# Optimization experiments

Hardware: AMD Instinct MI355X
Metric: run time of the kernel (lower is better)

## Reference

```python
import jax, jax.numpy as jnp
import numpy as np

HIDDEN_DIM = 640
VOCAB_SIZE = 1024


def setup_inputs() -> dict:
    key = jax.random.key(0)
    kf, kp, kw, kb = jax.random.split(key, 4)
    B, T, U, H, V = 8, 256, 64, HIDDEN_DIM, VOCAB_SIZE
    f = jax.random.normal(kf, (B, T, H), dtype=jnp.float32)
    p = jax.random.normal(kp, (B, U, H), dtype=jnp.float32)
    # nn.Linear default init: U(-1/sqrt(H), 1/sqrt(H))
    bound = 1.0 / np.sqrt(H)
    W = jax.random.uniform(kw, (V, H), minval=-bound, maxval=bound, dtype=jnp.float32)
    b = jax.random.uniform(kb, (V,), minval=-bound, maxval=bound, dtype=jnp.float32)
    return {"f": f, "p": p, "W": W, "b": b}


def reference(f, p, W, b):
    # f: (B,T,H), p: (B,U,H) -> combined: (B,T,U,H)
    combined = f[:, :, None, :] + p[:, None, :, :]
    h = jax.nn.relu(combined)
    # Linear: h @ W^T + b -> (B,T,U,V)
    logits = jnp.einsum('btuh,vh->btuv', h, W) + b
    return logits
```

## Files before the change

### kernel.cpp

```cpp
#include <hip/hip_runtime.h>
#include <hip/hip_bf16.h>

#define BDIM 8
#define TDIM 256
#define UDIM 64
#define HDIM 640
#define VDIM 1024
#define MDIM (BDIM * TDIM * UDIM)

#define BM 128
#define BN 128
#define BK 32
#define NT (HDIM / BK)

typedef __attribute__((ext_vector_type(8))) short short8;
typedef __attribute__((ext_vector_type(4))) float f32x4;

__device__ __forceinline__ ushort f2bf(float x) {
    union { float f; unsigned int u; } v; v.f = x;
    unsigned int r = (v.u + 0x7fffu + ((v.u >> 16) & 1u)) >> 16;
    return (ushort)r;
}

__global__ void cvt_w_kernel(const float* __restrict__ W, ushort* __restrict__ Wb) {
    int i = (blockIdx.x * 256 + threadIdx.x) * 4;
    f32x4 w = *(const f32x4*)(W + i);
    ushort4 o;
    o.x = f2bf(w[0]); o.y = f2bf(w[1]); o.z = f2bf(w[2]); o.w = f2bf(w[3]);
    *(ushort4*)(Wb + i) = o;
}

__global__ __launch_bounds__(256) void build_h_kernel(
    const float* __restrict__ f, const float* __restrict__ p,
    ushort* __restrict__ h)
{
    const int tid = threadIdx.x;
    const int row = (blockIdx.x << 5) + (tid >> 3);
    const int j0  = tid & 7;
    const int b = row >> 14;
    const int t = (row >> 6) & (TDIM - 1);
    const int u = row & (UDIM - 1);
    const float* frow = f + (size_t)(b * TDIM + t) * HDIM;
    const float* prow = p + (size_t)(b * UDIM + u) * HDIM;
    ushort* hrow = h + (size_t)row * HDIM;
    #pragma unroll
    for (int it = 0; it < HDIM / 64; ++it) {
        const int k = (j0 + it * 8) * 8;
        f32x4 f0 = *(const f32x4*)(frow + k);
        f32x4 f1 = *(const f32x4*)(frow + k + 4);
        f32x4 p0 = *(const f32x4*)(prow + k);
        f32x4 p1 = *(const f32x4*)(prow + k + 4);
        short8 hv;
        #pragma unroll
        for (int e = 0; e < 4; ++e) {
            float a0 = fmaxf(f0[e] + p0[e], 0.0f);
            float a1 = fmaxf(f1[e] + p1[e], 0.0f);
            hv[e]     = (short)f2bf(a0);
            hv[e + 4] = (short)f2bf(a1);
        }
        *(short8*)(hrow + k) = hv;
    }
}

#define GLDS(srcptr, ldsptr)                                                   \
    __builtin_amdgcn_global_load_lds(                                          \
        (const __attribute__((address_space(1))) void*)(srcptr),               \
        (__attribute__((address_space(3))) void*)(ldsptr), 16, 0, 0)

__global__ __launch_bounds__(256, 4) void hgemm128_kernel(
    const ushort* __restrict__ h,
    const ushort* __restrict__ Wb,
    const float* __restrict__ bias,
    float* __restrict__ out)
{
    __shared__ ushort Ash[2][BM * BK];
    __shared__ ushort Bsh[2][BN * BK];

    const int tid  = threadIdx.x;
    const int lane = tid & 63;
    const int wave = tid >> 6;
    const int wm   = wave >> 1;
    const int wn   = wave & 1;

    const int bid   = blockIdx.x;
    const int work  = (bid & 7) * 1024 + (bid >> 3);
    const int mtile = work >> 3;
    const int ntile = work & 7;
    const int m0 = mtile * BM;
    const int v0 = ntile * BN;

    const ushort* hbase = h  + (size_t)m0 * HDIM;
    const ushort* wbase = Wb + (size_t)v0 * HDIM;

    const int r0a = tid >> 2;
    const int r0b = r0a + 64;
    const int j0  = tid & 3;
    const size_t sof0 = (size_t)r0a * HDIM + (j0 ^ ((r0a >> 1) & 3)) * 8;
    const size_t sof1 = (size_t)r0b * HDIM + (j0 ^ ((r0b >> 1) & 3)) * 8;
    const int u0 = (wave * 64) * 8;
    const int u1 = (256 + wave * 64) * 8;

    int aoff[4], boff[4];
    #pragma unroll
    for (int mi = 0; mi < 4; ++mi) {
        const int r = wm * 64 + mi * 16 + (lane & 15);
        aoff[mi] = (r * 4 + ((lane >> 4) ^ ((r >> 1) & 3))) * 8;
    }
    #pragma unroll
    for (int ni = 0; ni < 4; ++ni) {
        const int r = wn * 64 + ni * 16 + (lane & 15);
        boff[ni] = (r * 4 + ((lane >> 4) ^ ((r >> 1) & 3))) * 8;
    }

    f32x4 acc[4][4];
    #pragma unroll
    for (int i = 0; i < 4; ++i)
        #pragma unroll
        for (int j = 0; j < 4; ++j)
            acc[i][j] = (f32x4)0.0f;

#define STG(kt, bf) do {                                                       \
        GLDS(hbase + sof0 + (kt) * BK, &Ash[bf][u0]);                          \
        GLDS(hbase + sof1 + (kt) * BK, &Ash[bf][u1]);                          \
        GLDS(wbase + sof0 + (kt) * BK, &Bsh[bf][u0]);                          \
        GLDS(wbase + sof1 + (kt) * BK, &Bsh[bf][u1]);                          \
    } while (0)

#define TILE(t, d) do {                                                        \
        if ((t) + 1 < NT) {                                                    \
            STG((t) + 1, (d) ^ 1);                                             \
            asm volatile("s_waitcnt vmcnt(4)" ::: "memory");                   \
        } else {                                                               \
            asm volatile("s_waitcnt vmcnt(0)" ::: "memory");                   \
        }                                                                      \
        __builtin_amdgcn_sched_barrier(0);                                     \
        __builtin_amdgcn_s_barrier();         \
        __builtin_amdgcn_sched_barrier(0);                                     \
        short8 afr[4], bfr[4];                                                 \
        _Pragma("unroll")                                                      \
        for (int q = 0; q < 4; ++q) {                                          \
            afr[q] = *(const short8*)(&Ash[d][aoff[q]]);                       \
            bfr[q] = *(const short8*)(&Bsh[d][boff[q]]);                       \
        }                                                                      \
        __builtin_amdgcn_s_setprio(1);                                         \
        _Pragma("unroll")                                                      \
        for (int mi = 0; mi < 4; ++mi)                                         \
            _Pragma("unroll")                                                  \
            for (int ni = 0; ni < 4; ++ni)                                     \
                acc[mi][ni] = __builtin_amdgcn_mfma_f32_16x16x32_bf16(         \
                    afr[mi], bfr[ni], acc[mi][ni], 0, 0, 0);                   \
        __builtin_amdgcn_s_setprio(0);                                         \
        __builtin_amdgcn_sched_barrier(0);                                     \
        __builtin_amdgcn_s_barrier();              \
    } while (0)

    STG(0, 0);
    #pragma unroll 1
    for (int t = 0; t < NT; t += 2) {
        TILE(t, 0);
        TILE(t + 1, 1);
    }
#undef TILE
#undef STG

    #pragma unroll
    for (int ni = 0; ni < 4; ++ni) {
        const int col = v0 + wn * 64 + ni * 16 + (lane & 15);
        const float bv = bias[col];
        #pragma unroll
        for (int mi = 0; mi < 4; ++mi) {
            const int rbase = m0 + wm * 64 + mi * 16 + ((lane >> 4) << 2);
            #pragma unroll
            for (int reg = 0; reg < 4; ++reg) {
                out[(size_t)(rbase + reg) * VDIM + col] = acc[mi][ni][reg] + bv;
            }
        }
    }
}

template <bool USE_WB>
__global__ __launch_bounds__(256) void joint_gemm_kernel(
    const float* __restrict__ f, const float* __restrict__ p,
    const float* __restrict__ Wf, const ushort* __restrict__ Wb,
    const float* __restrict__ bias, float* __restrict__ out)
{
    __shared__ ushort Alds[128 * 64];
    __shared__ ushort Blds[128 * 64];

    const int tid  = threadIdx.x;
    const int lane = tid & 63;
    const int wave = tid >> 6;
    const int wm   = wave >> 1;
    const int wn   = wave & 1;

    const int bid   = blockIdx.x;
    const int work  = (bid & 7) * 1024 + (bid >> 3);
    const int mtile = work >> 3;
    const int ntile = work & 7;
    const int m0 = mtile * 128;
    const int v0 = ntile * 128;

    const int b  = m0 >> 14;
    const int t0 = (m0 >> 6) & (TDIM - 1);

    const float*  fbase = f + (size_t)(b * TDIM + t0) * HDIM;
    const float*  pbase = p + (size_t)b * UDIM * HDIM;
    const ushort* wbbase = Wb + (size_t)v0 * HDIM;
    const float*  wfbase = Wf + (size_t)v0 * HDIM;

    f32x4 acc[4][4];
    #pragma unroll
    for (int i = 0; i < 4; ++i)
        #pragma unroll
        for (int j = 0; j < 4; ++j)
            acc[i][j] = (f32x4)0.0f;

    for (int kt = 0; kt < HDIM / 64; ++kt) {
        const int k0 = kt * 64;
        __syncthreads();

        if (USE_WB) {
            #pragma unroll
            for (int it = 0; it < 4; ++it) {
                const int c   = it * 256 + tid;
                const int row = c >> 3;
                const int j   = c & 7;
                const ushort* src = wbbase + row * HDIM + k0 + ((j ^ (row & 7)) << 3);
                GLDS(src, &Blds[(it * 256 + wave * 64) * 8]);
            }
        } else {
            #pragma unroll
            for (int it = 0; it < 4; ++it) {
                const int c   = it * 256 + tid;
                const int row = c >> 3;
                const int j   = c & 7;
                const float* wp = wfbase + row * HDIM + k0 + j * 8;
                f32x4 w0 = *(const f32x4*)wp;
                f32x4 w1 = *(const f32x4*)(wp + 4);
                short8 wv;
                #pragma unroll
                for (int e = 0; e < 4; ++e) {
                    wv[e]     = (short)f2bf(w0[e]);
                    wv[e + 4] = (short)f2bf(w1[e]);
                }
                *(short8*)(&Blds[(row * 8 + (j ^ (row & 7))) * 8]) = wv;
            }
        }

        #pragma unroll
        for (int it = 0; it < 4; ++it) {
            const int c   = it * 256 + tid;
            const int row = c >> 3;
            const int j   = c & 7;
            const float* fp_ = fbase + (row >> 6) * HDIM + k0 + j * 8;
            const float* pp_ = pbase + (row & 63) * HDIM + k0 + j * 8;
            f32x4 f0 = *(const f32x4*)fp_;
            f32x4 f1 = *(const f32x4*)(fp_ + 4);
            f32x4 p0 = *(const f32x4*)pp_;
            f32x4 p1 = *(const f32x4*)(pp_ + 4);
            short8 hv;
            #pragma unroll
            for (int e = 0; e < 4; ++e) {
                float a0 = fmaxf(f0[e] + p0[e], 0.0f);
                float a1 = fmaxf(f1[e] + p1[e], 0.0f);
                hv[e]     = (short)f2bf(a0);
                hv[e + 4] = (short)f2bf(a1);
            }
            *(short8*)(&Alds[(row * 8 + (j ^ (row & 7))) * 8]) = hv;
        }

        __syncthreads();

        #pragma unroll
        for (int ks = 0; ks < 2; ++ks) {
            short8 afr[4], bfr[4];
            #pragma unroll
            for (int mi = 0; mi < 4; ++mi) {
                const int r = wm * 64 + mi * 16 + (lane & 15);
                const int j = ks * 4 + (lane >> 4);
                afr[mi] = *(const short8*)(&Alds[(r * 8 + (j ^ (r & 7))) * 8]);
            }
            #pragma unroll
            for (int ni = 0; ni < 4; ++ni) {
                const int r = wn * 64 + ni * 16 + (lane & 15);
                const int j = ks * 4 + (lane >> 4);
                bfr[ni] = *(const short8*)(&Blds[(r * 8 + (j ^ (r & 7))) * 8]);
            }
            #pragma unroll
            for (int mi = 0; mi < 4; ++mi)
                #pragma unroll
                for (int ni = 0; ni < 4; ++ni)
                    acc[mi][ni] = __builtin_amdgcn_mfma_f32_16x16x32_bf16(
                        afr[mi], bfr[ni], acc[mi][ni], 0, 0, 0);
        }
    }

    #pragma unroll
    for (int ni = 0; ni < 4; ++ni) {
        const int col = v0 + wn * 64 + ni * 16 + (lane & 15);
        const float bv = bias[col];
        #pragma unroll
        for (int mi = 0; mi < 4; ++mi) {
            const int rbase = m0 + wm * 64 + mi * 16 + ((lane >> 4) << 2);
            #pragma unroll
            for (int reg = 0; reg < 4; ++reg) {
                out[(size_t)(rbase + reg) * VDIM + col] = acc[mi][ni][reg] + bv;
            }
        }
    }
}

extern "C" void kernel_launch(void* const* d_in, const int* in_sizes, int n_in,
                              void* d_out, int out_size, void* d_ws, size_t ws_size,
                              hipStream_t stream) {
    const float* f    = (const float*)d_in[0];
    const float* p    = (const float*)d_in[1];
    const float* W    = (const float*)d_in[2];
    const float* bias = (const float*)d_in[3];
    float* out = (float*)d_out;

    const size_t wb_bytes = (size_t)VDIM * HDIM * sizeof(ushort);
    const size_t h_bytes  = (size_t)MDIM * HDIM * sizeof(ushort);

    if (ws_size >= wb_bytes + h_bytes) {
        ushort* Wb = (ushort*)d_ws;
        ushort* h  = (ushort*)((char*)d_ws + wb_bytes);
        cvt_w_kernel<<<(VDIM * HDIM) / 1024, 256, 0, stream>>>(W, Wb);
        build_h_kernel<<<MDIM / 32, 256, 0, stream>>>(f, p, h);
        const int grid = (MDIM / BM) * (VDIM / BN);
        hgemm128_kernel<<<grid, 256, 0, stream>>>(h, Wb, bias, out);
    } else if (ws_size >= wb_bytes) {
        ushort* Wb = (ushort*)d_ws;
        cvt_w_kernel<<<(VDIM * HDIM) / 1024, 256, 0, stream>>>(W, Wb);
        joint_gemm_kernel<true><<<(MDIM / 128) * (VDIM / 128), 256, 0, stream>>>(
            f, p, W, Wb, bias, out);
    } else {
        joint_gemm_kernel<false><<<(MDIM / 128) * (VDIM / 128), 256, 0, stream>>>(
            f, p, W, nullptr, bias, out);
    }
}
```

Before: 352.0 us.

## Triple-buffer LDS tiles with prefetch distance two and one barrier per step

The GEMM main loop now uses three LDS buffers instead of two. Global-to-LDS loads for tile t+2 are issued after the fragments for tile t have been read from LDS. This removes the second workgroup barrier in each k-step and lengthens the window in which loads can overlap MFMA work. The cost is 50% more LDS per block, and launch bounds are lowered from 4 to 3 blocks per CU, so occupancy may drop.

```diff
diff --git a/kernel.cpp b/kernel.cpp
--- a/kernel.cpp
+++ b/kernel.cpp
@@ -12,6 +12,7 @@
 #define BN 128
 #define BK 32
 #define NT (HDIM / BK)
+#define NBUF 3
 
 typedef __attribute__((ext_vector_type(8))) short short8;
 typedef __attribute__((ext_vector_type(4))) float f32x4;
@@ -67,14 +68,14 @@
         (const __attribute__((address_space(1))) void*)(srcptr),               \
         (__attribute__((address_space(3))) void*)(ldsptr), 16, 0, 0)
 
-__global__ __launch_bounds__(256, 4) void hgemm128_kernel(
+__global__ __launch_bounds__(256, 3) void hgemm128_kernel(
     const ushort* __restrict__ h,
     const ushort* __restrict__ Wb,
     const float* __restrict__ bias,
     float* __restrict__ out)
 {
-    __shared__ ushort Ash[2][BM * BK];
-    __shared__ ushort Bsh[2][BN * BK];
+    __shared__ ushort Ash[NBUF][BM * BK];
+    __shared__ ushort Bsh[NBUF][BN * BK];
 
     const int tid  = threadIdx.x;
     const int lane = tid & 63;
@@ -126,41 +127,41 @@
         GLDS(wbase + sof1 + (kt) * BK, &Bsh[bf][u1]);                          \
     } while (0)
 
-#define TILE(t, d) do {                                                        \
-        if ((t) + 1 < NT) {                                                    \
-            STG((t) + 1, (d) ^ 1);                                             \
-            asm volatile("s_waitcnt vmcnt(4)" ::: "memory");                   \
-        } else {                                                               \
-            asm volatile("s_waitcnt vmcnt(0)" ::: "memory");                   \
-        }                                                                      \
-        __builtin_amdgcn_sched_barrier(0);                                     \
-        __builtin_amdgcn_s_barrier();         \
-        __builtin_amdgcn_sched_barrier(0);                                     \
-        short8 afr[4], bfr[4];                                                 \
-        _Pragma("unroll")                                                      \
-        for (int q = 0; q < 4; ++q) {                                          \
-            afr[q] = *(const short8*)(&Ash[d][aoff[q]]);                       \
-            bfr[q] = *(const short8*)(&Bsh[d][boff[q]]);                       \
-        }                                                                      \
-        __builtin_amdgcn_s_setprio(1);                                         \
-        _Pragma("unroll")                                                      \
-        for (int mi = 0; mi < 4; ++mi)                                         \
-            _Pragma("unroll")                                                  \
-            for (int ni = 0; ni < 4; ++ni)                                     \
-                acc[mi][ni] = __builtin_amdgcn_mfma_f32_16x16x32_bf16(         \
-                    afr[mi], bfr[ni], acc[mi][ni], 0, 0, 0);                   \
-        __builtin_amdgcn_s_setprio(0);                                         \
-        __builtin_amdgcn_sched_barrier(0);                                     \
-        __builtin_amdgcn_s_barrier();              \
-    } while (0)
-
     STG(0, 0);
+    STG(1, 1);
+
+    int d = 0;
+    int e = 2;
     #pragma unroll 1
-    for (int t = 0; t < NT; t += 2) {
-        TILE(t, 0);
-        TILE(t + 1, 1);
-    }
-#undef TILE
+    for (int t = 0; t < NT; ++t) {
+        if (t < NT - 1) { asm volatile("s_waitcnt vmcnt(4)" ::: "memory"); }
+        else            { asm volatile("s_waitcnt vmcnt(0)" ::: "memory"); }
+        __builtin_amdgcn_sched_barrier(0);
+        __builtin_amdgcn_s_barrier();
+        __builtin_amdgcn_sched_barrier(0);
+
+        short8 afr[4], bfr[4];
+        #pragma unroll
+        for (int q = 0; q < 4; ++q) {
+            afr[q] = *(const short8*)(&Ash[d][aoff[q]]);
+            bfr[q] = *(const short8*)(&Bsh[d][boff[q]]);
+        }
+
+        if (t + 2 < NT) STG(t + 2, e);
+
+        __builtin_amdgcn_s_setprio(1);
+        #pragma unroll
+        for (int mi = 0; mi < 4; ++mi)
+            #pragma unroll
+            for (int ni = 0; ni < 4; ++ni)
+                acc[mi][ni] = __builtin_amdgcn_mfma_f32_16x16x32_bf16(
+                    afr[mi], bfr[ni], acc[mi][ni], 0, 0, 0);
+        __builtin_amdgcn_s_setprio(0);
+        __builtin_amdgcn_sched_barrier(0);
+
+        d = (d == NBUF - 1) ? 0 : d + 1;
+        e = (e == NBUF - 1) ? 0 : e + 1;
+    }
 #undef STG
 
     #pragma unroll
```

Result: slower. 376.4 us (+6.9%).

## Replace LDS-staged bf16 GEMM with register-direct double-buffered loads

Applied to the files above, without the earlier changes.

Swaps the LDS-staged GEMM for one where every wave loads its MFMA operand fragments straight from global memory into registers. Loads are double-buffered in registers, and all block barriers and shared-memory traffic are gone. The block tile grows to 128x256, with each wave owning a 128x64 output tile. The trade-off is that all four waves fetch the same A rows, so A is read four times per block, and the per-row 64-byte reads coalesce worse. Register pressure also rises, with occupancy capped at 2 blocks per CU.

```diff
diff --git a/kernel.cpp b/kernel.cpp
--- a/kernel.cpp
+++ b/kernel.cpp
@@ -8,8 +8,6 @@
 #define VDIM 1024
 #define MDIM (BDIM * TDIM * UDIM)
 
-#define BM 128
-#define BN 128
 #define BK 32
 #define NT (HDIM / BK)
 
@@ -62,114 +60,82 @@
     }
 }
 
-#define GLDS(srcptr, ldsptr)                                                   \
-    __builtin_amdgcn_global_load_lds(                                          \
-        (const __attribute__((address_space(1))) void*)(srcptr),               \
-        (__attribute__((address_space(3))) void*)(ldsptr), 16, 0, 0)
-
-__global__ __launch_bounds__(256, 4) void hgemm128_kernel(
+__global__ __launch_bounds__(256, 2) void hgemm_reg_kernel(
     const ushort* __restrict__ h,
     const ushort* __restrict__ Wb,
     const float* __restrict__ bias,
     float* __restrict__ out)
 {
-    __shared__ ushort Ash[2][BM * BK];
-    __shared__ ushort Bsh[2][BN * BK];
-
     const int tid  = threadIdx.x;
     const int lane = tid & 63;
     const int wave = tid >> 6;
-    const int wm   = wave >> 1;
-    const int wn   = wave & 1;
 
     const int bid   = blockIdx.x;
-    const int work  = (bid & 7) * 1024 + (bid >> 3);
-    const int mtile = work >> 3;
-    const int ntile = work & 7;
-    const int m0 = mtile * BM;
-    const int v0 = ntile * BN;
-
-    const ushort* hbase = h  + (size_t)m0 * HDIM;
-    const ushort* wbase = Wb + (size_t)v0 * HDIM;
-
-    const int r0a = tid >> 2;
-    const int r0b = r0a + 64;
-    const int j0  = tid & 3;
-    const size_t sof0 = (size_t)r0a * HDIM + (j0 ^ ((r0a >> 1) & 3)) * 8;
-    const size_t sof1 = (size_t)r0b * HDIM + (j0 ^ ((r0b >> 1) & 3)) * 8;
-    const int u0 = (wave * 64) * 8;
-    const int u1 = (256 + wave * 64) * 8;
-
-    int aoff[4], boff[4];
-    #pragma unroll
-    for (int mi = 0; mi < 4; ++mi) {
-        const int r = wm * 64 + mi * 16 + (lane & 15);
-        aoff[mi] = (r * 4 + ((lane >> 4) ^ ((r >> 1) & 3))) * 8;
-    }
-    #pragma unroll
-    for (int ni = 0; ni < 4; ++ni) {
-        const int r = wn * 64 + ni * 16 + (lane & 15);
-        boff[ni] = (r * 4 + ((lane >> 4) ^ ((r >> 1) & 3))) * 8;
-    }
-
-    f32x4 acc[4][4];
-    #pragma unroll
-    for (int i = 0; i < 4; ++i)
+    const int work  = (bid & 7) * 512 + (bid >> 3);
+    const int mtile = work >> 2;
+    const int ntile = work & 3;
+    const int m0 = mtile * 128;
+    const int v0 = ntile * 256 + wave * 64;
+
+    const int lr = lane & 15;
+    const int lk = (lane >> 4) * 8;
+
+    int aoffs[8], boffs[4];
+    #pragma unroll
+    for (int mi = 0; mi < 8; ++mi)
+        aoffs[mi] = (m0 + mi * 16 + lr) * HDIM + lk;
+    #pragma unroll
+    for (int ni = 0; ni < 4; ++ni)
+        boffs[ni] = (v0 + ni * 16 + lr) * HDIM + lk;
+
+    f32x4 acc[8][4];
+    #pragma unroll
+    for (int i = 0; i < 8; ++i)
         #pragma unroll
         for (int j = 0; j < 4; ++j)
             acc[i][j] = (f32x4)0.0f;
 
-#define STG(kt, bf) do {                                                       \
-        GLDS(hbase + sof0 + (kt) * BK, &Ash[bf][u0]);                          \
-        GLDS(hbase + sof1 + (kt) * BK, &Ash[bf][u1]);                          \
-        GLDS(wbase + sof0 + (kt) * BK, &Bsh[bf][u0]);                          \
-        GLDS(wbase + sof1 + (kt) * BK, &Bsh[bf][u1]);                          \
+    short8 a0[8], b0[4], a1[8], b1[4];
+
+#define LOADF(A, B, kt) do {                                                   \
+        const int koff_ = (kt) * BK;                                           \
+        _Pragma("unroll")                                                      \
+        for (int i_ = 0; i_ < 8; ++i_)                                         \
+            (A)[i_] = *(const short8*)(h + aoffs[i_] + koff_);                 \
+        _Pragma("unroll")                                                      \
+        for (int i_ = 0; i_ < 4; ++i_)                                         \
+            (B)[i_] = *(const short8*)(Wb + boffs[i_] + koff_);                \
     } while (0)
 
-#define TILE(t, d) do {                                                        \
-        if ((t) + 1 < NT) {                                                    \
-            STG((t) + 1, (d) ^ 1);                                             \
-            asm volatile("s_waitcnt vmcnt(4)" ::: "memory");                   \
-        } else {                                                               \
-            asm volatile("s_waitcnt vmcnt(0)" ::: "memory");                   \
-        }                                                                      \
-        __builtin_amdgcn_sched_barrier(0);                                     \
-        __builtin_amdgcn_s_barrier();         \
-        __builtin_amdgcn_sched_barrier(0);                                     \
-        short8 afr[4], bfr[4];                                                 \
-        _Pragma("unroll")                                                      \
-        for (int q = 0; q < 4; ++q) {                                          \
-            afr[q] = *(const short8*)(&Ash[d][aoff[q]]);                       \
-            bfr[q] = *(const short8*)(&Bsh[d][boff[q]]);                       \
-        }                                                                      \
+#define MFMAS(A, B) do {                                                       \
         __builtin_amdgcn_s_setprio(1);                                         \
         _Pragma("unroll")                                                      \
-        for (int mi = 0; mi < 4; ++mi)                                         \
+        for (int mi_ = 0; mi_ < 8; ++mi_)                                      \
             _Pragma("unroll")                                                  \
-            for (int ni = 0; ni < 4; ++ni)                                     \
-                acc[mi][ni] = __builtin_amdgcn_mfma_f32_16x16x32_bf16(         \
-                    afr[mi], bfr[ni], acc[mi][ni], 0, 0, 0);                   \
+            for (int ni_ = 0; ni_ < 4; ++ni_)                                  \
+                acc[mi_][ni_] = __builtin_amdgcn_mfma_f32_16x16x32_bf16(       \
+                    (A)[mi_], (B)[ni_], acc[mi_][ni_], 0, 0, 0);               \
         __builtin_amdgcn_s_setprio(0);                                         \
-        __builtin_amdgcn_sched_barrier(0);                                     \
-        __builtin_amdgcn_s_barrier();              \
     } while (0)
 
-    STG(0, 0);
+    LOADF(a0, b0, 0);
     #pragma unroll 1
     for (int t = 0; t < NT; t += 2) {
-        TILE(t, 0);
-        TILE(t + 1, 1);
-    }
-#undef TILE
-#undef STG
+        LOADF(a1, b1, t + 1);
+        MFMAS(a0, b0);
+        if (t + 2 < NT) LOADF(a0, b0, t + 2);
+        MFMAS(a1, b1);
+    }
+#undef LOADF
+#undef MFMAS
 
     #pragma unroll
     for (int ni = 0; ni < 4; ++ni) {
-        const int col = v0 + wn * 64 + ni * 16 + (lane & 15);
+        const int col = v0 + ni * 16 + lr;
         const float bv = bias[col];
         #pragma unroll
-        for (int mi = 0; mi < 4; ++mi) {
-            const int rbase = m0 + wm * 64 + mi * 16 + ((lane >> 4) << 2);
+        for (int mi = 0; mi < 8; ++mi) {
+            const int rbase = m0 + mi * 16 + ((lane >> 4) << 2);
             #pragma unroll
             for (int reg = 0; reg < 4; ++reg) {
                 out[(size_t)(rbase + reg) * VDIM + col] = acc[mi][ni][reg] + bv;
@@ -177,6 +143,11 @@
         }
     }
 }
+
+#define GLDS(srcptr, ldsptr)                                                   \
+    __builtin_amdgcn_global_load_lds(                                          \
+        (const __attribute__((address_space(1))) void*)(srcptr),               \
+        (__attribute__((address_space(3))) void*)(ldsptr), 16, 0, 0)
 
 template <bool USE_WB>
 __global__ __launch_bounds__(256) void joint_gemm_kernel(
@@ -327,8 +298,8 @@
         ushort* h  = (ushort*)((char*)d_ws + wb_bytes);
         cvt_w_kernel<<<(VDIM * HDIM) / 1024, 256, 0, stream>>>(W, Wb);
         build_h_kernel<<<MDIM / 32, 256, 0, stream>>>(f, p, h);
-        const int grid = (MDIM / BM) * (VDIM / BN);
-        hgemm128_kernel<<<grid, 256, 0, stream>>>(h, Wb, bias, out);
+        const int grid = (MDIM / 128) * (VDIM / 256);
+        hgemm_reg_kernel<<<grid, 256, 0, stream>>>(h, Wb, bias, out);
     } else if (ws_size >= wb_bytes) {
         ushort* Wb = (ushort*)d_ws;
         cvt_w_kernel<<<(VDIM * HDIM) / 1024, 256, 0, stream>>>(W, Wb);
```

After: 583.0 us. 65.6% more time.
